# Kernel optimization log

Hardware: AMD Instinct MI355X
Metric: run time of the kernel (lower is better)

Reference implementation:

```python
import jax, jax.numpy as jnp
import numpy as np

B, S, D = 2, 2048, 1024
H = 16
HD = D // H  # 64


def setup_inputs() -> dict:
    key = jax.random.key(0)
    ks = jax.random.split(key, 6)
    x = jax.random.normal(ks[0], (B, S, D), dtype=jnp.float32)
    sc = 1.0 / np.sqrt(D)
    Wq = jax.random.normal(ks[1], (D, D), dtype=jnp.float32) * sc
    Wk = jax.random.normal(ks[2], (D, D), dtype=jnp.float32) * sc
    Wv = jax.random.normal(ks[3], (D, D), dtype=jnp.float32) * sc
    Wo = jax.random.normal(ks[4], (D, D), dtype=jnp.float32) * sc
    bo = jax.random.normal(ks[5], (D,), dtype=jnp.float32) * 0.01
    return {"x": x, "Wq": Wq, "Wk": Wk, "Wv": Wv, "Wo": Wo, "bo": bo}


def reference(x, Wq, Wk, Wv, Wo, bo):
    b, s, d = x.shape
    # projections (torch Linear: y = x @ W.T; weights here stored as [d_in, d_out])
    Q = (x @ Wq).reshape(b, s, H, HD).transpose(0, 2, 1, 3)  # [b,h,s,hd]
    K = (x @ Wk).reshape(b, s, H, HD).transpose(0, 2, 1, 3)
    V = (x @ Wv).reshape(b, s, H, HD).transpose(0, 2, 1, 3)
    scores = jnp.einsum("bhqd,bhkd->bhqk", Q, K) / np.sqrt(HD)
    causal = jnp.triu(jnp.ones((s, s), dtype=bool), k=1)  # True above diagonal
    scores = jnp.where(causal[None, None], -jnp.inf, scores)
    attn = jax.nn.softmax(scores, axis=-1)
    # dropout_rate = 0.0 -> identity (eval-mode reference)
    ctx = jnp.einsum("bhqk,bhkd->bhqd", attn, V)
    ctx = ctx.transpose(0, 2, 1, 3).reshape(b, s, d)
    return ctx @ Wo + bo
```

## Files before the change

kernel.cpp:

```cpp
#include <hip/hip_runtime.h>
#include <hip/hip_bf16.h>

#define B_  2
#define S_  2048
#define D_  1024
#define H_  16
#define HD_ 64
#define M_  (B_*S_)

typedef __attribute__((ext_vector_type(8))) short short8;
typedef __attribute__((ext_vector_type(4))) float f32x4;

#define MFMA16(a, b, c) __builtin_amdgcn_mfma_f32_16x16x32_bf16((a), (b), (c), 0, 0, 0)

static __device__ inline short f2bf(float f) {
    union { float f; unsigned u; } v; v.f = f;
    unsigned r = v.u + 0x7FFFu + ((v.u >> 16) & 1u);
    return (short)(r >> 16);
}

static __device__ __forceinline__ float fexp2(float x) {
    float r;
    asm volatile("v_exp_f32 %0, %1\n\ts_nop 1" : "=v"(r) : "v"(x));
    return r;
}

static __device__ __forceinline__ unsigned cvt_pk_bf16(float lo, float hi) {
    unsigned r;
    asm volatile("v_cvt_pk_bf16_f32 %0, %1, %2" : "=v"(r) : "v"(lo), "v"(hi));
    return r;
}

static __device__ __forceinline__ void gl_lds16(const short* g, short* l) {
    __builtin_amdgcn_global_load_lds(
        (const __attribute__((address_space(1))) void*)g,
        (__attribute__((address_space(3))) void*)l, 16, 0, 0);
}

__global__ void cvt_x_kernel(const float* __restrict__ x, short* __restrict__ xb, int n4) {
    int i = blockIdx.x * blockDim.x + threadIdx.x;
    int stride = gridDim.x * blockDim.x;
    for (; i < n4; i += stride) {
        float4 v = ((const float4*)x)[i];
        short4 o;
        o.x = f2bf(v.x); o.y = f2bf(v.y); o.z = f2bf(v.z); o.w = f2bf(v.w);
        ((short4*)xb)[i] = o;
    }
}

__global__ void transpose_w_kernel(const float* __restrict__ W, short* __restrict__ Wt) {
    __shared__ float tile[32][33];
    int tx = threadIdx.x & 31, ty = threadIdx.x >> 5;
    int n0 = blockIdx.x * 32, k0 = blockIdx.y * 32;
#pragma unroll
    for (int i = 0; i < 4; ++i)
        tile[ty + 8 * i][tx] = W[(size_t)(k0 + ty + 8 * i) * D_ + n0 + tx];
    __syncthreads();
#pragma unroll
    for (int i = 0; i < 4; ++i)
        Wt[(size_t)(n0 + ty + 8 * i) * D_ + k0 + tx] = f2bf(tile[tx][ty + 8 * i]);
}

template <int MODE>
__global__ __launch_bounds__(256) void gemm128(const short* __restrict__ A,
                                               const short* __restrict__ Bt,
                                               const float* __restrict__ bias,
                                               void* __restrict__ out, int NB) {
    __shared__ __align__(16) short Asm[2][128 * 32];
    __shared__ __align__(16) short Bsm[2][128 * 32];
    int NBX = NB >> 3;
    int X = blockIdx.x & 7, t = blockIdx.x >> 3;
    int bm = t / NBX, bn = X * NBX + t % NBX;
    int tid = threadIdx.x, l = tid & 63, w = tid >> 6;
    int lhi = l >> 4, llo = l & 15;
    int wm = w >> 1, wn = w & 1;

    f32x4 acc[4][4];
#pragma unroll
    for (int m = 0; m < 4; ++m)
#pragma unroll
        for (int n = 0; n < 4; ++n) acc[m][n] = (f32x4){0.f, 0.f, 0.f, 0.f};

    const short* Ag = A + (size_t)(bm * 128) * 1024;
    const short* Bg = Bt + (size_t)(bn * 128) * 1024;
    int c0 = tid, c1 = 256 + tid;
    int r0 = ((c0 >> 5) << 3) | (c0 & 7), s0 = ((c0 >> 3) & 3) ^ (r0 & 3);
    int r1 = ((c1 >> 5) << 3) | (c1 & 7), s1 = ((c1 >> 3) & 3) ^ (r1 & 3);

    auto stage = [&](int buf, int k0) {
        gl_lds16(Ag + (size_t)r0 * 1024 + k0 + s0 * 8, &Asm[buf][c0 * 8]);
        gl_lds16(Ag + (size_t)r1 * 1024 + k0 + s1 * 8, &Asm[buf][c1 * 8]);
        gl_lds16(Bg + (size_t)r0 * 1024 + k0 + s0 * 8, &Bsm[buf][c0 * 8]);
        gl_lds16(Bg + (size_t)r1 * 1024 + k0 + s1 * 8, &Bsm[buf][c1 * 8]);
    };

    int cia[4], cib[4];
#pragma unroll
    for (int m = 0; m < 4; ++m) {
        int row = wm * 64 + m * 16 + llo;
        cia[m] = ((row >> 3) << 5) | (((lhi ^ row) & 3) << 3) | (row & 7);
    }
#pragma unroll
    for (int n = 0; n < 4; ++n) {
        int row = wn * 64 + n * 16 + llo;
        cib[n] = ((row >> 3) << 5) | (((lhi ^ row) & 3) << 3) | (row & 7);
    }

    stage(0, 0);
    for (int i = 0; i < 32; ++i) {
        asm volatile("s_waitcnt vmcnt(0)" ::: "memory");
        __builtin_amdgcn_s_barrier();
        asm volatile("" ::: "memory");
        if (i + 1 < 32) stage((i + 1) & 1, (i + 1) * 32);
        int cur = i & 1;
        short8 af[4], bf[4];
#pragma unroll
        for (int m = 0; m < 4; ++m) af[m] = *(const short8*)&Asm[cur][cia[m] * 8];
#pragma unroll
        for (int n = 0; n < 4; ++n) bf[n] = *(const short8*)&Bsm[cur][cib[n] * 8];
#pragma unroll
        for (int m = 0; m < 4; ++m)
#pragma unroll
            for (int n = 0; n < 4; ++n)
                acc[m][n] = MFMA16(af[m], bf[n], acc[m][n]);
    }

    int rowb = bm * 128 + wm * 64, colb = bn * 128 + wn * 64;
#pragma unroll
    for (int m = 0; m < 4; ++m) {
#pragma unroll
        for (int n = 0; n < 4; ++n) {
            int col = colb + n * 16 + llo;
#pragma unroll
            for (int j = 0; j < 4; ++j) {
                int row = rowb + m * 16 + lhi * 4 + j;
                float v = acc[m][n][j];
                if (MODE == 2) {
                    ((float*)out)[(size_t)row * 1024 + col] = v + bias[col];
                } else {
                    int proj = col >> 10, n1 = col & 1023;
                    int h = n1 >> 6, hd = n1 & 63;
                    int b = row >> 11, s = row & 2047;
                    short* o = (short*)out;
                    size_t off;
                    if (proj == 0)
                        off = ((size_t)(b * 16 + h) * 2048 + s) * 64 + hd;
                    else if (proj == 1)
                        off = (size_t)M_ * D_ + ((size_t)(b * 16 + h) * 2048 + s) * 64 + hd;
                    else
                        off = (size_t)2 * M_ * D_ + ((size_t)(b * 16 + h) * 64 + hd) * 2048 + s;
                    o[off] = f2bf(v);
                }
            }
        }
    }
}

__global__ __launch_bounds__(512) void attn_kernel(const short* __restrict__ Q,
                                                   const short* __restrict__ Kg,
                                                   const short* __restrict__ Vt,
                                                   short* __restrict__ ctx) {
    __shared__ __align__(16) char kvbuf[2][16384];
    __shared__ __align__(16) char plds[8][2048];
    int tid = threadIdx.x, w = tid >> 6, l = tid & 63;
    int lhi = l >> 4, llo = l & 15;
    int bh = blockIdx.x & 31, qp = blockIdx.x >> 5;
    int b = bh >> 4, h = bh & 15;
    char* pb = plds[w];

    const short* Qh = Q + (size_t)bh * S_ * HD_;
    const short* Kh = Kg + (size_t)bh * S_ * HD_;
    const short* Vh = Vt + (size_t)bh * HD_ * S_;

    int qbA = qp, qbB = 15 - qp;
    int NTA = 2 * qp + 2;
    const int NT = 34;

    int srow = tid >> 3;
    int ssrc = (16 * (tid & 7)) ^ ((srow & 7) << 4);
    auto stage = [&](char* buf, int c0) {
        gl_lds16(Kh + (size_t)(c0 + srow) * HD_ + (ssrc >> 1), (short*)(buf + tid * 16));
        gl_lds16(Vh + (size_t)srow * S_ + c0 + (ssrc >> 1), (short*)(buf + 8192 + tid * 16));
    };

    f32x4 O[4];
#pragma unroll
    for (int n = 0; n < 4; ++n) O[n] = (f32x4){0.f, 0.f, 0.f, 0.f};
    float lpart[4] = {0.f, 0.f, 0.f, 0.f};

    auto writeOut = [&](int qb) {
        int qbs = qb * 128 + w * 16;
#pragma unroll
        for (int j = 0; j < 4; ++j) {
            float ls = lpart[j];
            ls += __shfl_xor(ls, 1);
            ls += __shfl_xor(ls, 2);
            ls += __shfl_xor(ls, 4);
            ls += __shfl_xor(ls, 8);
            float inv = 1.0f / ls;
            int row = qbs + lhi * 4 + j;
            size_t base = ((size_t)(b * S_ + row)) * D_ + h * HD_;
#pragma unroll
            for (int n = 0; n < 4; ++n)
                ctx[base + n * 16 + llo] = f2bf(O[n][j] * inv);
        }
    };

    const float SC = 0.18033688f;
    const float M2 = 17.312340f;

    int qbase = qbA * 128 + w * 16;
    short8 aq0 = *(const short8*)(Qh + (size_t)(qbase + llo) * HD_ + 8 * lhi);
    short8 aq1 = *(const short8*)(Qh + (size_t)(qbase + llo) * HD_ + 32 + 8 * lhi);

    stage(kvbuf[0], 0);

    for (int i = 0; i < NT; ++i) {
        asm volatile("s_waitcnt vmcnt(0)" ::: "memory");
        __builtin_amdgcn_s_barrier();
        asm volatile("" ::: "memory");
        int kt = (i < NTA) ? i : i - NTA;
        int c0 = kt * 64;
        if (i + 1 < NT) {
            int ni = i + 1;
            int nkt = (ni < NTA) ? ni : ni - NTA;
            stage(kvbuf[ni & 1], nkt * 64);
        }
        const char* kb = kvbuf[i & 1];
        const char* vb = kb + 8192;

        if (c0 <= qbase + 15) {
            f32x4 sc4[4];
#pragma unroll
            for (int cb = 0; cb < 4; ++cb) {
                int row = cb * 16 + llo;
                int sw = (row & 7) << 4;
                short8 kf0 = *(const short8*)(kb + row * 128 + ((16 * lhi) ^ sw));
                short8 kf1 = *(const short8*)(kb + row * 128 + ((64 + 16 * lhi) ^ sw));
                f32x4 z = (f32x4){0.f, 0.f, 0.f, 0.f};
                z = MFMA16(aq0, kf0, z);
                z = MFMA16(aq1, kf1, z);
                sc4[cb] = z;
            }
            bool diag = (c0 + 63 > qbase);
#pragma unroll
            for (int j = 0; j < 4; ++j) {
                int qr = qbase + lhi * 4 + j;
                float v0 = fmaf(sc4[0][j], SC, -M2);
                float v1 = fmaf(sc4[1][j], SC, -M2);
                float v2 = fmaf(sc4[2][j], SC, -M2);
                float v3 = fmaf(sc4[3][j], SC, -M2);
                if (diag) {
                    if (c0 + llo > qr)      v0 = -1e30f;
                    if (c0 + 16 + llo > qr) v1 = -1e30f;
                    if (c0 + 32 + llo > qr) v2 = -1e30f;
                    if (c0 + 48 + llo > qr) v3 = -1e30f;
                }
                float p0 = fexp2(v0), p1 = fexp2(v1);
                float p2 = fexp2(v2), p3 = fexp2(v3);
                lpart[j] += (p0 + p1) + (p2 + p3);
                unsigned pk01 = cvt_pk_bf16(p0, p1);
                unsigned pk23 = cvt_pk_bf16(p2, p3);
                int r = lhi * 4 + j;
                char* rb = pb + r * 128;
                int sw = (r & 7) << 4;
                *(short*)(rb + ((2 * llo) ^ sw))      = (short)(pk01);
                *(short*)(rb + ((2 * llo + 32) ^ sw)) = (short)(pk01 >> 16);
                *(short*)(rb + ((2 * llo + 64) ^ sw)) = (short)(pk23);
                *(short*)(rb + ((2 * llo + 96) ^ sw)) = (short)(pk23 >> 16);
            }
            int swr = (llo & 7) << 4;
            short8 pa0 = *(const short8*)(pb + llo * 128 + ((16 * lhi) ^ swr));
            short8 pa1 = *(const short8*)(pb + llo * 128 + ((64 + 16 * lhi) ^ swr));
#pragma unroll
            for (int n = 0; n < 4; ++n) {
                int row = n * 16 + llo;
                int sw = (row & 7) << 4;
                short8 vf0 = *(const short8*)(vb + row * 128 + ((16 * lhi) ^ sw));
                short8 vf1 = *(const short8*)(vb + row * 128 + ((64 + 16 * lhi) ^ sw));
                O[n] = MFMA16(pa0, vf0, O[n]);
                O[n] = MFMA16(pa1, vf1, O[n]);
            }
        }

        if (i == NTA - 1) {
            writeOut(qbA);
#pragma unroll
            for (int n = 0; n < 4; ++n) O[n] = (f32x4){0.f, 0.f, 0.f, 0.f};
            lpart[0] = lpart[1] = lpart[2] = lpart[3] = 0.f;
            qbase = qbB * 128 + w * 16;
            aq0 = *(const short8*)(Qh + (size_t)(qbase + llo) * HD_ + 8 * lhi);
            aq1 = *(const short8*)(Qh + (size_t)(qbase + llo) * HD_ + 32 + 8 * lhi);
        }
    }
    writeOut(qbB);
}

extern "C" void kernel_launch(void* const* d_in, const int* in_sizes, int n_in,
                              void* d_out, int out_size, void* d_ws, size_t ws_size,
                              hipStream_t stream) {
    const float* x  = (const float*)d_in[0];
    const float* Wq = (const float*)d_in[1];
    const float* Wk = (const float*)d_in[2];
    const float* Wv = (const float*)d_in[3];
    const float* Wo = (const float*)d_in[4];
    const float* bo = (const float*)d_in[5];
    float* out = (float*)d_out;

    char* ws = (char*)d_ws;
    short* xb    = (short*)(ws);
    short* Wqkvt = (short*)(ws + (size_t)(8 << 20));
    short* Wot   = (short*)(ws + (size_t)(14 << 20));
    short* Qb    = (short*)(ws + (size_t)(16 << 20));
    short* Kb    = Qb + (size_t)M_ * D_;
    short* Vtb   = Qb + (size_t)2 * M_ * D_;
    short* ctx   = xb;

    cvt_x_kernel<<<2048, 256, 0, stream>>>(x, xb, M_ * D_ / 4);
    dim3 tg(32, 32);
    transpose_w_kernel<<<tg, 256, 0, stream>>>(Wq, Wqkvt);
    transpose_w_kernel<<<tg, 256, 0, stream>>>(Wk, Wqkvt + (1 << 20));
    transpose_w_kernel<<<tg, 256, 0, stream>>>(Wv, Wqkvt + (2 << 20));
    transpose_w_kernel<<<tg, 256, 0, stream>>>(Wo, Wot);

    gemm128<0><<<32 * 24, 256, 0, stream>>>(xb, Wqkvt, nullptr, Qb, 24);
    attn_kernel<<<256, 512, 0, stream>>>(Qb, Kb, Vtb, ctx);
    gemm128<2><<<32 * 8, 256, 0, stream>>>(ctx, Wot, bo, out, 8);
}
```

Before: 146.6 us.

## Triple-buffer GEMM and attention K/V loads and merge weight transposes into one launch

The GEMM and attention kernels move from double to triple buffering in LDS. Each now prefetches two tiles ahead and waits with partial vmcnt counts instead of draining all outstanding loads every iteration, so global-to-LDS latency overlaps more compute. The four weight-transpose launches are also folded into a single 3D-grid launch, removing kernel launch overhead. The extra LDS per block (GEMM grows to 48KB, attention to 64KB) may cut occupancy, and the partial waits depend on exact per-thread load counts being correct.

```diff
diff --git a/kernel.cpp b/kernel.cpp
--- a/kernel.cpp
+++ b/kernel.cpp
@@ -48,8 +48,13 @@
     }
 }
 
-__global__ void transpose_w_kernel(const float* __restrict__ W, short* __restrict__ Wt) {
+__global__ void transpose_w4_kernel(const float* __restrict__ Wq, const float* __restrict__ Wk,
+                                    const float* __restrict__ Wv, const float* __restrict__ Wo,
+                                    short* __restrict__ Wqkvt, short* __restrict__ Wot) {
     __shared__ float tile[32][33];
+    int z = blockIdx.z;
+    const float* W = (z == 0) ? Wq : (z == 1) ? Wk : (z == 2) ? Wv : Wo;
+    short* Wt = (z == 3) ? Wot : (Wqkvt + ((size_t)z << 20));
     int tx = threadIdx.x & 31, ty = threadIdx.x >> 5;
     int n0 = blockIdx.x * 32, k0 = blockIdx.y * 32;
 #pragma unroll
@@ -66,8 +71,8 @@
                                                const short* __restrict__ Bt,
                                                const float* __restrict__ bias,
                                                void* __restrict__ out, int NB) {
-    __shared__ __align__(16) short Asm[2][128 * 32];
-    __shared__ __align__(16) short Bsm[2][128 * 32];
+    __shared__ __align__(16) short Asm[3][128 * 32];
+    __shared__ __align__(16) short Bsm[3][128 * 32];
     int NBX = NB >> 3;
     int X = blockIdx.x & 7, t = blockIdx.x >> 3;
     int bm = t / NBX, bn = X * NBX + t % NBX;
@@ -107,12 +112,13 @@
     }
 
     stage(0, 0);
+    stage(1, 32);
     for (int i = 0; i < 32; ++i) {
-        asm volatile("s_waitcnt vmcnt(0)" ::: "memory");
+        if (i < 30) { asm volatile("s_waitcnt vmcnt(4)" ::: "memory"); }
+        else        { asm volatile("s_waitcnt vmcnt(0)" ::: "memory"); }
         __builtin_amdgcn_s_barrier();
-        asm volatile("" ::: "memory");
-        if (i + 1 < 32) stage((i + 1) & 1, (i + 1) * 32);
-        int cur = i & 1;
+        if (i + 2 < 32) stage((i + 2) % 3, (i + 2) * 32);
+        int cur = i % 3;
         short8 af[4], bf[4];
 #pragma unroll
         for (int m = 0; m < 4; ++m) af[m] = *(const short8*)&Asm[cur][cia[m] * 8];
@@ -160,7 +166,7 @@
                                                    const short* __restrict__ Kg,
                                                    const short* __restrict__ Vt,
                                                    short* __restrict__ ctx) {
-    __shared__ __align__(16) char kvbuf[2][16384];
+    __shared__ __align__(16) char kvbuf[3][16384];
     __shared__ __align__(16) char plds[8][2048];
     int tid = threadIdx.x, w = tid >> 6, l = tid & 63;
     int lhi = l >> 4, llo = l & 15;
@@ -175,6 +181,8 @@
     int qbA = qp, qbB = 15 - qp;
     int NTA = 2 * qp + 2;
     const int NT = 34;
+
+    auto tileof = [&](int i) { return (i < NTA) ? i : i - NTA; };
 
     int srow = tid >> 3;
     int ssrc = (16 * (tid & 7)) ^ ((srow & 7) << 4);
@@ -213,20 +221,16 @@
     short8 aq0 = *(const short8*)(Qh + (size_t)(qbase + llo) * HD_ + 8 * lhi);
     short8 aq1 = *(const short8*)(Qh + (size_t)(qbase + llo) * HD_ + 32 + 8 * lhi);
 
-    stage(kvbuf[0], 0);
+    stage(kvbuf[0], tileof(0) * 64);
+    stage(kvbuf[1], tileof(1) * 64);
 
     for (int i = 0; i < NT; ++i) {
-        asm volatile("s_waitcnt vmcnt(0)" ::: "memory");
+        if (i < NT - 2) { asm volatile("s_waitcnt vmcnt(2)" ::: "memory"); }
+        else            { asm volatile("s_waitcnt vmcnt(0)" ::: "memory"); }
         __builtin_amdgcn_s_barrier();
-        asm volatile("" ::: "memory");
-        int kt = (i < NTA) ? i : i - NTA;
-        int c0 = kt * 64;
-        if (i + 1 < NT) {
-            int ni = i + 1;
-            int nkt = (ni < NTA) ? ni : ni - NTA;
-            stage(kvbuf[ni & 1], nkt * 64);
-        }
-        const char* kb = kvbuf[i & 1];
+        if (i + 2 < NT) stage(kvbuf[(i + 2) % 3], tileof(i + 2) * 64);
+        int c0 = tileof(i) * 64;
+        const char* kb = kvbuf[i % 3];
         const char* vb = kb + 8192;
 
         if (c0 <= qbase + 15) {
@@ -317,11 +321,7 @@
     short* ctx   = xb;
 
     cvt_x_kernel<<<2048, 256, 0, stream>>>(x, xb, M_ * D_ / 4);
-    dim3 tg(32, 32);
-    transpose_w_kernel<<<tg, 256, 0, stream>>>(Wq, Wqkvt);
-    transpose_w_kernel<<<tg, 256, 0, stream>>>(Wk, Wqkvt + (1 << 20));
-    transpose_w_kernel<<<tg, 256, 0, stream>>>(Wv, Wqkvt + (2 << 20));
-    transpose_w_kernel<<<tg, 256, 0, stream>>>(Wo, Wot);
+    transpose_w4_kernel<<<dim3(32, 32, 4), 256, 0, stream>>>(Wq, Wk, Wv, Wo, Wqkvt, Wot);
 
     gemm128<0><<<32 * 24, 256, 0, stream>>>(xb, Wqkvt, nullptr, Qb, 24);
     attn_kernel<<<256, 512, 0, stream>>>(Qb, Kb, Vtb, ctx);
```

After: 150.7 us. +2.8%, slower.

## Split-K the output projection GEMM and merge weight transpose launches

Applied to the files above, without the earlier changes.

The output projection GEMM now splits K in two, launching twice as many blocks. Each half writes its partial result to the output or to a scratch buffer that reuses the dead Q region, and a separate kernel sums the two and adds the bias. The four weight-transpose launches are also merged into one launch using a z grid dimension. The aim is to fill more CUs during the output GEMM and cut launch overhead, at the cost of extra memory traffic and an additional kernel launch.

```diff
diff --git a/kernel.cpp b/kernel.cpp
--- a/kernel.cpp
+++ b/kernel.cpp
@@ -48,8 +48,13 @@
     }
 }
 
-__global__ void transpose_w_kernel(const float* __restrict__ W, short* __restrict__ Wt) {
+__global__ void transpose_w4_kernel(const float* __restrict__ Wq, const float* __restrict__ Wk,
+                                    const float* __restrict__ Wv, const float* __restrict__ Wo,
+                                    short* __restrict__ Wqkvt, short* __restrict__ Wot) {
     __shared__ float tile[32][33];
+    int z = blockIdx.z;
+    const float* W = (z == 0) ? Wq : (z == 1) ? Wk : (z == 2) ? Wv : Wo;
+    short* Wt = (z == 3) ? Wot : (Wqkvt + ((size_t)z << 20));
     int tx = threadIdx.x & 31, ty = threadIdx.x >> 5;
     int n0 = blockIdx.x * 32, k0 = blockIdx.y * 32;
 #pragma unroll
@@ -61,16 +66,35 @@
         Wt[(size_t)(n0 + ty + 8 * i) * D_ + k0 + tx] = f2bf(tile[tx][ty + 8 * i]);
 }
 
+__global__ void reduce_bias_kernel(float* __restrict__ out, const float* __restrict__ p1,
+                                   const float* __restrict__ bias, int n4) {
+    int i = blockIdx.x * blockDim.x + threadIdx.x;
+    int stride = gridDim.x * blockDim.x;
+    for (; i < n4; i += stride) {
+        float4 a = ((const float4*)out)[i];
+        float4 b = ((const float4*)p1)[i];
+        float4 c = ((const float4*)bias)[i & 255];
+        a.x += b.x + c.x; a.y += b.y + c.y; a.z += b.z + c.z; a.w += b.w + c.w;
+        ((float4*)out)[i] = a;
+    }
+}
+
 template <int MODE>
 __global__ __launch_bounds__(256) void gemm128(const short* __restrict__ A,
                                                const short* __restrict__ Bt,
-                                               const float* __restrict__ bias,
+                                               float* __restrict__ pscr,
                                                void* __restrict__ out, int NB) {
     __shared__ __align__(16) short Asm[2][128 * 32];
     __shared__ __align__(16) short Bsm[2][128 * 32];
-    int NBX = NB >> 3;
     int X = blockIdx.x & 7, t = blockIdx.x >> 3;
-    int bm = t / NBX, bn = X * NBX + t % NBX;
+    int bm, bn, ks;
+    if (MODE == 0) {
+        int NBX = NB >> 3;
+        bm = t / NBX; bn = X * NBX + t % NBX; ks = 0;
+    } else {
+        ks = t & 1; bm = t >> 1; bn = X;
+    }
+    const int NSTEP = (MODE == 0) ? 32 : 16;
     int tid = threadIdx.x, l = tid & 63, w = tid >> 6;
     int lhi = l >> 4, llo = l & 15;
     int wm = w >> 1, wn = w & 1;
@@ -81,8 +105,8 @@
 #pragma unroll
         for (int n = 0; n < 4; ++n) acc[m][n] = (f32x4){0.f, 0.f, 0.f, 0.f};
 
-    const short* Ag = A + (size_t)(bm * 128) * 1024;
-    const short* Bg = Bt + (size_t)(bn * 128) * 1024;
+    const short* Ag = A + (size_t)(bm * 128) * 1024 + ks * 512;
+    const short* Bg = Bt + (size_t)(bn * 128) * 1024 + ks * 512;
     int c0 = tid, c1 = 256 + tid;
     int r0 = ((c0 >> 5) << 3) | (c0 & 7), s0 = ((c0 >> 3) & 3) ^ (r0 & 3);
     int r1 = ((c1 >> 5) << 3) | (c1 & 7), s1 = ((c1 >> 3) & 3) ^ (r1 & 3);
@@ -107,11 +131,11 @@
     }
 
     stage(0, 0);
-    for (int i = 0; i < 32; ++i) {
+    for (int i = 0; i < NSTEP; ++i) {
         asm volatile("s_waitcnt vmcnt(0)" ::: "memory");
         __builtin_amdgcn_s_barrier();
         asm volatile("" ::: "memory");
-        if (i + 1 < 32) stage((i + 1) & 1, (i + 1) * 32);
+        if (i + 1 < NSTEP) stage((i + 1) & 1, (i + 1) * 32);
         int cur = i & 1;
         short8 af[4], bf[4];
 #pragma unroll
@@ -136,7 +160,8 @@
                 int row = rowb + m * 16 + lhi * 4 + j;
                 float v = acc[m][n][j];
                 if (MODE == 2) {
-                    ((float*)out)[(size_t)row * 1024 + col] = v + bias[col];
+                    float* o = ks ? pscr : (float*)out;
+                    o[(size_t)row * 1024 + col] = v;
                 } else {
                     int proj = col >> 10, n1 = col & 1023;
                     int h = n1 >> 6, hd = n1 & 63;
@@ -315,15 +340,13 @@
     short* Kb    = Qb + (size_t)M_ * D_;
     short* Vtb   = Qb + (size_t)2 * M_ * D_;
     short* ctx   = xb;
+    float* pscr  = (float*)(ws + (size_t)(16 << 20));
 
     cvt_x_kernel<<<2048, 256, 0, stream>>>(x, xb, M_ * D_ / 4);
-    dim3 tg(32, 32);
-    transpose_w_kernel<<<tg, 256, 0, stream>>>(Wq, Wqkvt);
-    transpose_w_kernel<<<tg, 256, 0, stream>>>(Wk, Wqkvt + (1 << 20));
-    transpose_w_kernel<<<tg, 256, 0, stream>>>(Wv, Wqkvt + (2 << 20));
-    transpose_w_kernel<<<tg, 256, 0, stream>>>(Wo, Wot);
+    transpose_w4_kernel<<<dim3(32, 32, 4), 256, 0, stream>>>(Wq, Wk, Wv, Wo, Wqkvt, Wot);
 
     gemm128<0><<<32 * 24, 256, 0, stream>>>(xb, Wqkvt, nullptr, Qb, 24);
     attn_kernel<<<256, 512, 0, stream>>>(Qb, Kb, Vtb, ctx);
-    gemm128<2><<<32 * 8, 256, 0, stream>>>(ctx, Wot, bo, out, 8);
-}
+    gemm128<2><<<512, 256, 0, stream>>>(ctx, Wot, pscr, out, 8);
+    reduce_bias_kernel<<<2048, 256, 0, stream>>>(out, pscr, bo, M_ * D_ / 4);
+}
```

Result: faster. 139.6 us (-4.7%).

## Shrink GEMM tiles to 64x128 for more blocks and merge weight transposes

Applied to the files above, without the earlier changes.

Replaces the 128x128-tile GEMM with a 64x128-tile variant, where each wave computes a 64x32 slice. This doubles the number of workgroups so the 256-CU GPU is better filled: the output projection goes from 256 to 512 blocks. It also sets launch bounds for higher occupancy and remaps blocks to tiles. The four weight-transpose launches are fused into one 3D-grid launch to cut launch overhead. Smaller tiles reduce data reuse per block and raise the LDS and global traffic per FLOP.

```diff
diff --git a/kernel.cpp b/kernel.cpp
--- a/kernel.cpp
+++ b/kernel.cpp
@@ -48,8 +48,13 @@
     }
 }
 
-__global__ void transpose_w_kernel(const float* __restrict__ W, short* __restrict__ Wt) {
+__global__ void transpose_w4_kernel(const float* __restrict__ Wq, const float* __restrict__ Wk,
+                                    const float* __restrict__ Wv, const float* __restrict__ Wo,
+                                    short* __restrict__ Wqkvt, short* __restrict__ Wot) {
     __shared__ float tile[32][33];
+    int z = blockIdx.z;
+    const float* W = (z == 0) ? Wq : (z == 1) ? Wk : (z == 2) ? Wv : Wo;
+    short* Wt = (z == 3) ? Wot : (Wqkvt + ((size_t)z << 20));
     int tx = threadIdx.x & 31, ty = threadIdx.x >> 5;
     int n0 = blockIdx.x * 32, k0 = blockIdx.y * 32;
 #pragma unroll
@@ -62,47 +67,48 @@
 }
 
 template <int MODE>
-__global__ __launch_bounds__(256) void gemm128(const short* __restrict__ A,
-                                               const short* __restrict__ Bt,
-                                               const float* __restrict__ bias,
-                                               void* __restrict__ out, int NB) {
-    __shared__ __align__(16) short Asm[2][128 * 32];
+__global__ __launch_bounds__(256, 6) void gemm64(const short* __restrict__ A,
+                                                 const short* __restrict__ Bt,
+                                                 const float* __restrict__ bias,
+                                                 void* __restrict__ out) {
+    __shared__ __align__(16) short Asm[2][64 * 32];
     __shared__ __align__(16) short Bsm[2][128 * 32];
-    int NBX = NB >> 3;
-    int X = blockIdx.x & 7, t = blockIdx.x >> 3;
-    int bm = t / NBX, bn = X * NBX + t % NBX;
+    int x = blockIdx.x & 7, wgl = blockIdx.x >> 3;
+    int bm, bn;
+    if (MODE == 0) { bn = x * 3 + (wgl >> 6); bm = wgl & 63; }
+    else           { bn = x;                  bm = wgl;      }
     int tid = threadIdx.x, l = tid & 63, w = tid >> 6;
     int lhi = l >> 4, llo = l & 15;
-    int wm = w >> 1, wn = w & 1;
-
-    f32x4 acc[4][4];
+
+    f32x4 acc[4][2];
 #pragma unroll
     for (int m = 0; m < 4; ++m)
 #pragma unroll
-        for (int n = 0; n < 4; ++n) acc[m][n] = (f32x4){0.f, 0.f, 0.f, 0.f};
-
-    const short* Ag = A + (size_t)(bm * 128) * 1024;
+        for (int n = 0; n < 2; ++n) acc[m][n] = (f32x4){0.f, 0.f, 0.f, 0.f};
+
+    const short* Ag = A + (size_t)(bm * 64) * 1024;
     const short* Bg = Bt + (size_t)(bn * 128) * 1024;
-    int c0 = tid, c1 = 256 + tid;
-    int r0 = ((c0 >> 5) << 3) | (c0 & 7), s0 = ((c0 >> 3) & 3) ^ (r0 & 3);
-    int r1 = ((c1 >> 5) << 3) | (c1 & 7), s1 = ((c1 >> 3) & 3) ^ (r1 & 3);
+    int ca = tid;
+    int ra = ((ca >> 5) << 3) | (ca & 7), sa = ((ca >> 3) & 3) ^ (ra & 3);
+    int cb0 = tid, cb1 = tid + 256;
+    int rb0 = ((cb0 >> 5) << 3) | (cb0 & 7), sb0 = ((cb0 >> 3) & 3) ^ (rb0 & 3);
+    int rb1 = ((cb1 >> 5) << 3) | (cb1 & 7), sb1 = ((cb1 >> 3) & 3) ^ (rb1 & 3);
 
     auto stage = [&](int buf, int k0) {
-        gl_lds16(Ag + (size_t)r0 * 1024 + k0 + s0 * 8, &Asm[buf][c0 * 8]);
-        gl_lds16(Ag + (size_t)r1 * 1024 + k0 + s1 * 8, &Asm[buf][c1 * 8]);
-        gl_lds16(Bg + (size_t)r0 * 1024 + k0 + s0 * 8, &Bsm[buf][c0 * 8]);
-        gl_lds16(Bg + (size_t)r1 * 1024 + k0 + s1 * 8, &Bsm[buf][c1 * 8]);
+        gl_lds16(Ag + (size_t)ra * 1024 + k0 + sa * 8, &Asm[buf][ca * 8]);
+        gl_lds16(Bg + (size_t)rb0 * 1024 + k0 + sb0 * 8, &Bsm[buf][cb0 * 8]);
+        gl_lds16(Bg + (size_t)rb1 * 1024 + k0 + sb1 * 8, &Bsm[buf][cb1 * 8]);
     };
 
-    int cia[4], cib[4];
+    int cia[4], cib[2];
 #pragma unroll
     for (int m = 0; m < 4; ++m) {
-        int row = wm * 64 + m * 16 + llo;
+        int row = m * 16 + llo;
         cia[m] = ((row >> 3) << 5) | (((lhi ^ row) & 3) << 3) | (row & 7);
     }
 #pragma unroll
-    for (int n = 0; n < 4; ++n) {
-        int row = wn * 64 + n * 16 + llo;
+    for (int n = 0; n < 2; ++n) {
+        int row = w * 32 + n * 16 + llo;
         cib[n] = ((row >> 3) << 5) | (((lhi ^ row) & 3) << 3) | (row & 7);
     }
 
@@ -113,23 +119,23 @@
         asm volatile("" ::: "memory");
         if (i + 1 < 32) stage((i + 1) & 1, (i + 1) * 32);
         int cur = i & 1;
-        short8 af[4], bf[4];
+        short8 af[4], bf[2];
 #pragma unroll
         for (int m = 0; m < 4; ++m) af[m] = *(const short8*)&Asm[cur][cia[m] * 8];
 #pragma unroll
-        for (int n = 0; n < 4; ++n) bf[n] = *(const short8*)&Bsm[cur][cib[n] * 8];
+        for (int n = 0; n < 2; ++n) bf[n] = *(const short8*)&Bsm[cur][cib[n] * 8];
 #pragma unroll
         for (int m = 0; m < 4; ++m)
 #pragma unroll
-            for (int n = 0; n < 4; ++n)
+            for (int n = 0; n < 2; ++n)
                 acc[m][n] = MFMA16(af[m], bf[n], acc[m][n]);
     }
 
-    int rowb = bm * 128 + wm * 64, colb = bn * 128 + wn * 64;
+    int rowb = bm * 64, colb = bn * 128 + w * 32;
 #pragma unroll
     for (int m = 0; m < 4; ++m) {
 #pragma unroll
-        for (int n = 0; n < 4; ++n) {
+        for (int n = 0; n < 2; ++n) {
             int col = colb + n * 16 + llo;
 #pragma unroll
             for (int j = 0; j < 4; ++j) {
@@ -317,13 +323,9 @@
     short* ctx   = xb;
 
     cvt_x_kernel<<<2048, 256, 0, stream>>>(x, xb, M_ * D_ / 4);
-    dim3 tg(32, 32);
-    transpose_w_kernel<<<tg, 256, 0, stream>>>(Wq, Wqkvt);
-    transpose_w_kernel<<<tg, 256, 0, stream>>>(Wk, Wqkvt + (1 << 20));
-    transpose_w_kernel<<<tg, 256, 0, stream>>>(Wv, Wqkvt + (2 << 20));
-    transpose_w_kernel<<<tg, 256, 0, stream>>>(Wo, Wot);
-
-    gemm128<0><<<32 * 24, 256, 0, stream>>>(xb, Wqkvt, nullptr, Qb, 24);
+    transpose_w4_kernel<<<dim3(32, 32, 4), 256, 0, stream>>>(Wq, Wk, Wv, Wo, Wqkvt, Wot);
+
+    gemm64<0><<<1536, 256, 0, stream>>>(xb, Wqkvt, nullptr, Qb);
     attn_kernel<<<256, 512, 0, stream>>>(Qb, Kb, Vtb, ctx);
-    gemm128<2><<<32 * 8, 256, 0, stream>>>(ctx, Wot, bo, out, 8);
-}
+    gemm64<2><<<512, 256, 0, stream>>>(ctx, Wot, bo, out);
+}
```

Result: faster. 140.2 us (-4.3%).
